# Kernel optimization log

Hardware: AMD Instinct MI355X
Metric: run time of the kernel (lower is better)

## Reference

```python
import jax, jax.numpy as jnp
import numpy as np

NUM_COLS = 8      # MyTopoAgent.num_columns
NUM_SELECTED = 4  # MyTopoAgent.num_selected


def _gatv2(x, src, tgt, Wl, bl, Wr, br, att, bias, n):
    """PyG GATv2Conv (share_weights=False, concat=True, negative_slope=0.2).
    x: [n, Din]; src/tgt: [E] (self loops already appended); att: [H, C]."""
    H, C = att.shape
    xl = (x @ Wl + bl).reshape(n, H, C)   # lin_l(x) -> source transform
    xr = (x @ Wr + br).reshape(n, H, C)   # lin_r(x) -> target transform
    # e_ij = att . leaky_relu(xl[j] + xr[i])  per head
    e = jnp.einsum('ehc,hc->eh', jax.nn.leaky_relu(xl[src] + xr[tgt], 0.2), att)  # [E, H]
    # segment softmax over edges sharing a target node (stable via segment max)
    m = jax.lax.stop_gradient(jax.ops.segment_max(e, tgt, num_segments=n))
    ex = jnp.exp(e - m[tgt])
    denom = jax.ops.segment_sum(ex, tgt, num_segments=n)
    alpha = ex / (denom[tgt] + 1e-16)
    out = jax.ops.segment_sum(xl[src] * alpha[..., None], tgt, num_segments=n)  # [n, H, C]
    return out.reshape(n, H * C) + bias


def setup_inputs() -> dict:
    key = jax.random.key(0)
    B, N, D, Hd, Ch, E = 4, 10000, 128, 128, 7, 640000
    M = B * N
    ks = iter(jax.random.split(key, 40))
    nx = lambda shape: jax.random.normal(next(ks), shape, dtype=jnp.float32) * 0.05
    inp = {}
    inp['x'] = jax.random.normal(next(ks), (B, N, D), dtype=jnp.float32)
    inp['edge_index'] = jax.random.randint(next(ks), (2, E), 0, M)
    inp['gumbel_u'] = jax.random.uniform(next(ks), (B, NUM_COLS, Ch), dtype=jnp.float32,
                                         minval=1e-6, maxval=1.0 - 1e-6)
    # actor gat1(D->Hd), actor gat2(Hd->Ch), critic gat1(D->Hd), critic gat2(Hd->Hd); heads=1
    for pre, di, do in (('a1', D, Hd), ('a2', Hd, Ch), ('c1', D, Hd), ('c2', Hd, Hd)):
        inp[pre + '_Wl'] = nx((di, do))
        inp[pre + '_bl'] = jnp.zeros((do,), jnp.float32)
        inp[pre + '_Wr'] = nx((di, do))
        inp[pre + '_br'] = jnp.zeros((do,), jnp.float32)
        inp[pre + '_att'] = nx((1, do))
        inp[pre + '_b'] = jnp.zeros((do,), jnp.float32)
    inp['fc_W'] = nx((Hd, 1))
    inp['fc_b'] = jnp.zeros((1,), jnp.float32)
    return inp


def reference(x, edge_index, gumbel_u,
              a1_Wl, a1_bl, a1_Wr, a1_br, a1_att, a1_b,
              a2_Wl, a2_bl, a2_Wr, a2_br, a2_att, a2_b,
              c1_Wl, c1_bl, c1_Wr, c1_br, c1_att, c1_b,
              c2_Wl, c2_bl, c2_Wr, c2_br, c2_att, c2_b,
              fc_W, fc_b):
    B, N, D = x.shape
    M = B * N
    xf = x.reshape(M, D)
    loops = jnp.arange(M, dtype=edge_index.dtype)  # PyG add_self_loops
    src = jnp.concatenate([edge_index[0], loops])
    tgt = jnp.concatenate([edge_index[1], loops])
    # ---- actor: GATv2 -> leaky_relu(0.01) -> GATv2 -> softmax ----
    h = _gatv2(xf, src, tgt, a1_Wl, a1_bl, a1_Wr, a1_br, a1_att, a1_b, M)
    h = jax.nn.leaky_relu(h, 0.01)
    logits = _gatv2(h, src, tgt, a2_Wl, a2_bl, a2_Wr, a2_br, a2_att, a2_b, M).reshape(B, N, -1)
    probs = jax.nn.softmax(logits, axis=-1)  # [B, N, 7]
    # multinomial(k=4, no replacement) per column via Gumbel top-k
    g = -jnp.log(-jnp.log(gumbel_u))                       # [B, 8, 7]
    scores = jnp.log(probs[:, :NUM_COLS, :]) + g
    _, action = jax.lax.top_k(scores, NUM_SELECTED)        # [B, 8, 4]
    # torch gather(dim=1): sel[b,i,j] = probs[b, action[b,i,j], j]
    sel = probs[jnp.arange(B)[:, None, None], action, jnp.arange(NUM_SELECTED)[None, None, :]]
    # ---- critic: GATv2 -> leaky_relu(0.01) -> GATv2 -> Linear ----
    hc = _gatv2(xf, src, tgt, c1_Wl, c1_bl, c1_Wr, c1_br, c1_att, c1_b, M)
    hc = jax.nn.leaky_relu(hc, 0.01)
    hc = _gatv2(hc, src, tgt, c2_Wl, c2_bl, c2_Wr, c2_br, c2_att, c2_b, M).reshape(B, N, -1)
    value = hc @ fc_W + fc_b  # [B, N, 1]
    return action, sel, value
```

## Files before the change

kernel.cpp:

```cpp
#include <hip/hip_runtime.h>
#include <math.h>


typedef __attribute__((ext_vector_type(8))) short bf16x8;
typedef __attribute__((ext_vector_type(4))) float f32x4;

__device__ __forceinline__ float wave_reduce_sum(float v){
  #pragma unroll
  for (int o = 32; o > 0; o >>= 1) v += __shfl_xor(v, o);
  return v;
}
__device__ __forceinline__ unsigned short f2bf(float f){
  unsigned int u = __float_as_uint(f);
  u += 0x7FFFu + ((u >> 16) & 1u);
  return (unsigned short)(u >> 16);
}
__device__ __forceinline__ void unpack2(unsigned int u, float& a, float& b){
  a = __uint_as_float(u << 16);
  b = __uint_as_float(u & 0xffff0000u);
}

__global__ void k_zero(int* __restrict__ p, int n){
  int i = blockIdx.x * blockDim.x + threadIdx.x;
  if (i < n) p[i] = 0;
}

__global__ void k_scatter(const int* __restrict__ ei, int E,
                          int* __restrict__ cnt, int* __restrict__ bucket,
                          const float* __restrict__ W1l, const float* __restrict__ W1r,
                          const float* __restrict__ W2l, const float* __restrict__ W2r,
                          unsigned short* __restrict__ Wt1, unsigned short* __restrict__ Wt2){
  int e = blockIdx.x * blockDim.x + threadIdx.x;
  if (e < E){
    int s = ei[e], t = ei[E + e];
    int pos = atomicAdd(&cnt[t], 1);
    if (pos < 64) bucket[(size_t)t * 64 + pos] = s;
  } else {
    int r = e - E;
    if (r < 65536){
      int which = r >> 15;
      int lin = r & 32767;
      const float* Wl = which ? W2l : W1l;
      const float* Wr = which ? W2r : W1r;
      unsigned short* Wt = which ? Wt2 : Wt1;
      int n = lin >> 7, k = lin & 127;
      float v = (n < 128) ? Wl[(size_t)k * 128 + n] : Wr[(size_t)k * 128 + (n - 128)];
      Wt[lin] = f2bf(v);
    }
  }
}

__device__ __forceinline__ void dev_mark1(
    const int* __restrict__ cnt, const int* __restrict__ bucket,
    int* __restrict__ flag1, int* __restrict__ list1, int* __restrict__ n1, int N){
  int p = threadIdx.x;
  if (p >= 32) return;
  int node = (p >> 3) * N + (p & 7);
  if (atomicExch(&flag1[node], 1) == 0) list1[atomicAdd(n1, 1)] = node;
  int deg = min(cnt[node], 64);
  const int* crow = bucket + (size_t)node * 64;
  for (int j = 0; j < deg; ++j){
    int s = crow[j];
    if (atomicExch(&flag1[s], 1) == 0) list1[atomicAdd(n1, 1)] = s;
  }
}
__device__ __forceinline__ void dev_mark2(
    int vbid, int nblk,
    const int* __restrict__ cnt, const int* __restrict__ bucket,
    const int* __restrict__ list1, const int* __restrict__ n1,
    int* __restrict__ flag2, int* __restrict__ list2, int* __restrict__ n2){
  int n = *n1;
  for (int i = vbid * blockDim.x + threadIdx.x; i < n; i += nblk * blockDim.x){
    int node = list1[i];
    if (atomicExch(&flag2[node], 1) == 0) list2[atomicAdd(n2, 1)] = node;
    int deg = min(cnt[node], 64);
    const int* crow = bucket + (size_t)node * 64;
    for (int j = 0; j < deg; ++j){
      int s = crow[j];
      if (atomicExch(&flag2[s], 1) == 0) list2[atomicAdd(n2, 1)] = s;
    }
  }
}

__device__ __forceinline__ void dev_gemm_dual(
    int bid, const float* __restrict__ A,
    const float* __restrict__ Wl, const float* __restrict__ Wr,
    const float* __restrict__ blv, const float* __restrict__ brv,
    float* __restrict__ XL1, float* __restrict__ XR1,
    const int* __restrict__ list1, const int* __restrict__ list2,
    const int* __restrict__ nn,
    float (*As)[17], float (*Ws)[64]){
  const float* W; const float* bias; float* Out; const int* rows; int n;
  int colBase, bx, nbx;
  if (bid < 384){
    W = Wl; bias = blv; Out = XL1; rows = list2; n = nn[1];
    colBase = (bid / 192) * 64; bx = bid % 192; nbx = 192;
  } else {
    int rem = bid - 384;
    W = Wr; bias = brv; Out = XR1; rows = list1; n = nn[0];
    colBase = (rem / 64) * 64; bx = rem % 64; nbx = 64;
  }
  int tid = threadIdx.x;
  int tx = tid & 15, ty = tid >> 4;
  int ar = tid >> 2, ac = (tid & 3) << 2;
  int kr = tid >> 4, nc = (tid & 15) << 2;
  for (int base = bx * 64; base < n; base += nbx * 64){
    float acc[4][4] = {};
    int arow = rows[min(base + ar, n - 1)];
    for (int k0 = 0; k0 < 128; k0 += 16){
      float4 av = *(const float4*)(A + (size_t)arow * 128 + k0 + ac);
      As[ar][ac + 0] = av.x; As[ar][ac + 1] = av.y;
      As[ar][ac + 2] = av.z; As[ar][ac + 3] = av.w;
      float4 wv = *(const float4*)(W + (size_t)(k0 + kr) * 128 + colBase + nc);
      *(float4*)&Ws[kr][nc] = wv;
      __syncthreads();
      #pragma unroll
      for (int kk = 0; kk < 16; ++kk){
        float a0 = As[ty * 4 + 0][kk];
        float a1 = As[ty * 4 + 1][kk];
        float a2 = As[ty * 4 + 2][kk];
        float a3 = As[ty * 4 + 3][kk];
        float4 b = *(const float4*)&Ws[kk][tx * 4];
        acc[0][0] += a0 * b.x; acc[0][1] += a0 * b.y; acc[0][2] += a0 * b.z; acc[0][3] += a0 * b.w;
        acc[1][0] += a1 * b.x; acc[1][1] += a1 * b.y; acc[1][2] += a1 * b.z; acc[1][3] += a1 * b.w;
        acc[2][0] += a2 * b.x; acc[2][1] += a2 * b.y; acc[2][2] += a2 * b.z; acc[2][3] += a2 * b.w;
        acc[3][0] += a3 * b.x; acc[3][1] += a3 * b.y; acc[3][2] += a3 * b.z; acc[3][3] += a3 * b.w;
      }
      __syncthreads();
    }
    int cN = colBase + tx * 4;
    float4 bb = *(const float4*)(bias + cN);
    #pragma unroll
    for (int i = 0; i < 4; ++i){
      int r = rows[min(base + ty * 4 + i, n - 1)];
      float4 o;
      o.x = acc[i][0] + bb.x; o.y = acc[i][1] + bb.y;
      o.z = acc[i][2] + bb.z; o.w = acc[i][3] + bb.w;
      *(float4*)(Out + (size_t)r * 128 + cN) = o;
    }
  }
}

template<bool CVT>
__device__ __forceinline__ void dev_gemm_mfma(
    int rblk, const void* __restrict__ Av, const unsigned short* __restrict__ Wt,
    const float* __restrict__ bl, const float* __restrict__ br,
    unsigned short* __restrict__ XL, unsigned short* __restrict__ XR){
  int w = threadIdx.x >> 6, lane = threadIdx.x & 63;
  int l16 = lane & 15, kg = lane >> 4;
  int rBase = rblk * 64 + w * 16;
  f32x4 acc[16];
  #pragma unroll
  for (int i = 0; i < 16; ++i) acc[i] = (f32x4){0.f, 0.f, 0.f, 0.f};
  #pragma unroll
  for (int ks = 0; ks < 4; ++ks){
    bf16x8 a;
    if constexpr (CVT){
      const float* A = (const float*)Av;
      const float* ap = A + (size_t)(rBase + l16) * 128 + ks * 32 + kg * 8;
      float4 f0 = *(const float4*)ap;
      float4 f1 = *(const float4*)(ap + 4);
      union { bf16x8 v; unsigned short s[8]; } u;
      u.s[0] = f2bf(f0.x); u.s[1] = f2bf(f0.y); u.s[2] = f2bf(f0.z); u.s[3] = f2bf(f0.w);
      u.s[4] = f2bf(f1.x); u.s[5] = f2bf(f1.y); u.s[6] = f2bf(f1.z); u.s[7] = f2bf(f1.w);
      a = u.v;
    } else {
      a = *(const bf16x8*)((const unsigned short*)Av + (size_t)(rBase + l16) * 128 + ks * 32 + kg * 8);
    }
    #pragma unroll
    for (int ct = 0; ct < 16; ++ct){
      bf16x8 wv = *(const bf16x8*)(Wt + (size_t)(ct * 16 + l16) * 128 + ks * 32 + kg * 8);
      acc[ct] = __builtin_amdgcn_mfma_f32_16x16x32_bf16(wv, a, acc[ct], 0, 0, 0);
    }
  }
  int row = rBase + l16;
  #pragma unroll
  for (int ct = 0; ct < 16; ++ct){
    int col = ct * 16 + kg * 4;
    const float* bp = (col < 128) ? (bl + col) : (br + (col - 128));
    float4 bb = *(const float4*)bp;
    unsigned int p0 = (unsigned int)f2bf(acc[ct][0] + bb.x) |
                      ((unsigned int)f2bf(acc[ct][1] + bb.y) << 16);
    unsigned int p1 = (unsigned int)f2bf(acc[ct][2] + bb.z) |
                      ((unsigned int)f2bf(acc[ct][3] + bb.w) << 16);
    unsigned short* dst = (col < 128) ? (XL + (size_t)row * 128 + col)
                                      : (XR + (size_t)row * 128 + (col - 128));
    uint2 pk; pk.x = p0; pk.y = p1;
    *(uint2*)dst = pk;
  }
}

template<int MODE>
__device__ __forceinline__ void dev_gather16(
    int gid, int l,
    const unsigned short* __restrict__ XL, const unsigned short* __restrict__ XR,
    const int* __restrict__ cnt, const int* __restrict__ bucket,
    const float* __restrict__ att, const float* __restrict__ bias,
    const float* __restrict__ fcW, const float* __restrict__ fcb,
    void* __restrict__ outp){
  uint4 xu = *(const uint4*)(XR + (size_t)gid * 128 + l * 8);
  float xr[8];
  unpack2(xu.x, xr[0], xr[1]); unpack2(xu.y, xr[2], xr[3]);
  unpack2(xu.z, xr[4], xr[5]); unpack2(xu.w, xr[6], xr[7]);
  float at[8];
  {
    float4 a0 = *(const float4*)(att + l * 8);
    float4 a1 = *(const float4*)(att + l * 8 + 4);
    at[0] = a0.x; at[1] = a0.y; at[2] = a0.z; at[3] = a0.w;
    at[4] = a1.x; at[5] = a1.y; at[6] = a1.z; at[7] = a1.w;
  }
  int deg = min(cnt[gid], 64);
  const int* __restrict__ crow = bucket + (size_t)gid * 64;
  float m = -INFINITY, den = 0.f;
  float acc[8] = {0.f, 0.f, 0.f, 0.f, 0.f, 0.f, 0.f, 0.f};

  auto proc = [&](uint4 u){
    float xl[8];
    unpack2(u.x, xl[0], xl[1]); unpack2(u.y, xl[2], xl[3]);
    unpack2(u.z, xl[4], xl[5]); unpack2(u.w, xl[6], xl[7]);
    float e = 0.f;
    #pragma unroll
    for (int c = 0; c < 8; ++c){
      float v = xl[c] + xr[c];
      v = fmaxf(v, 0.2f * v);
      e = fmaf(v, at[c], e);
    }
    e += __shfl_xor(e, 1, 16);
    e += __shfl_xor(e, 2, 16);
    e += __shfl_xor(e, 4, 16);
    e += __shfl_xor(e, 8, 16);
    if (e > m){
      float sc = __expf(m - e);
      den *= sc;
      #pragma unroll
      for (int c = 0; c < 8; ++c) acc[c] *= sc;
      m = e;
    }
    float p = __expf(e - m);
    den += p;
    #pragma unroll
    for (int c = 0; c < 8; ++c) acc[c] = fmaf(p, xl[c], acc[c]);
  };

  proc(*(const uint4*)(XL + (size_t)gid * 128 + l * 8));

  int nq = deg >> 2;
  int j = 0;
  if (nq > 0){
    uint4 r0, r1, r2, r3;
    {
      int s0 = crow[0], s1 = crow[1], s2 = crow[2], s3 = crow[3];
      r0 = *(const uint4*)(XL + (size_t)s0 * 128 + l * 8);
      r1 = *(const uint4*)(XL + (size_t)s1 * 128 + l * 8);
      r2 = *(const uint4*)(XL + (size_t)s2 * 128 + l * 8);
      r3 = *(const uint4*)(XL + (size_t)s3 * 128 + l * 8);
    }
    for (int q = 1;; ++q){
      bool more = (q < nq);
      uint4 n0, n1, n2, n3;
      if (more){
        int b4 = q * 4;
        int t0 = crow[b4 + 0], t1 = crow[b4 + 1], t2 = crow[b4 + 2], t3 = crow[b4 + 3];
        n0 = *(const uint4*)(XL + (size_t)t0 * 128 + l * 8);
        n1 = *(const uint4*)(XL + (size_t)t1 * 128 + l * 8);
        n2 = *(const uint4*)(XL + (size_t)t2 * 128 + l * 8);
        n3 = *(const uint4*)(XL + (size_t)t3 * 128 + l * 8);
      }
      proc(r0); proc(r1); proc(r2); proc(r3);
      if (!more) break;
      r0 = n0; r1 = n1; r2 = n2; r3 = n3;
    }
    j = nq * 4;
  }
  for (; j < deg; ++j){
    int s = crow[j];
    proc(*(const uint4*)(XL + (size_t)s * 128 + l * 8));
  }

  float r = 1.f / (den + 1e-16f);
  float4 b0 = *(const float4*)(bias + l * 8);
  float4 b1 = *(const float4*)(bias + l * 8 + 4);
  float o[8];
  o[0] = acc[0] * r + b0.x; o[1] = acc[1] * r + b0.y;
  o[2] = acc[2] * r + b0.z; o[3] = acc[3] * r + b0.w;
  o[4] = acc[4] * r + b1.x; o[5] = acc[5] * r + b1.y;
  o[6] = acc[6] * r + b1.z; o[7] = acc[7] * r + b1.w;
  if (MODE == 0){
    #pragma unroll
    for (int c = 0; c < 8; ++c) o[c] = o[c] > 0.f ? o[c] : 0.01f * o[c];
    uint4 pk;
    pk.x = (unsigned int)f2bf(o[0]) | ((unsigned int)f2bf(o[1]) << 16);
    pk.y = (unsigned int)f2bf(o[2]) | ((unsigned int)f2bf(o[3]) << 16);
    pk.z = (unsigned int)f2bf(o[4]) | ((unsigned int)f2bf(o[5]) << 16);
    pk.w = (unsigned int)f2bf(o[6]) | ((unsigned int)f2bf(o[7]) << 16);
    *(uint4*)((unsigned short*)outp + (size_t)gid * 128 + l * 8) = pk;
  } else {
    float4 w0 = *(const float4*)(fcW + l * 8);
    float4 w1 = *(const float4*)(fcW + l * 8 + 4);
    float pv = o[0] * w0.x + o[1] * w0.y + o[2] * w0.z + o[3] * w0.w +
               o[4] * w1.x + o[5] * w1.y + o[6] * w1.z + o[7] * w1.w;
    pv += __shfl_xor(pv, 1, 16);
    pv += __shfl_xor(pv, 2, 16);
    pv += __shfl_xor(pv, 4, 16);
    pv += __shfl_xor(pv, 8, 16);
    if (l == 0) ((float*)outp)[gid] = pv + fcb[0];
  }
}

__device__ __forceinline__ void dev_a1_fused(
    int vbid,
    const float* __restrict__ XL, const float* __restrict__ XR,
    const int* __restrict__ cnt, const int* __restrict__ bucket,
    const float* __restrict__ att, const float* __restrict__ bias,
    const float* __restrict__ Wl7, const float* __restrict__ Wr7,
    const float* __restrict__ bl7, const float* __restrict__ br7,
    float* __restrict__ XL2, float* __restrict__ XR2,
    const int* __restrict__ list, const int* __restrict__ n_dev){
  int n = *n_dev;
  int lane = threadIdx.x & 63;
  const int wstride = (256 * 256) >> 6;
  for (int i = (vbid * 256 + (int)threadIdx.x) >> 6; i < n; i += wstride){
    int wid = list[i];
    float2 xr = ((const float2*)(XR + (size_t)wid * 128))[lane];
    float2 at = ((const float2*)att)[lane];
    int deg = min(cnt[wid], 64);
    const int* crow = bucket + (size_t)wid * 64;
    float m = -INFINITY, den = 0.f, acc0 = 0.f, acc1 = 0.f;
    for (int j = -1; j < deg; ++j){
      int s = (j < 0) ? wid : crow[j];
      float2 xl = ((const float2*)(XL + (size_t)s * 128))[lane];
      float v0 = xl.x + xr.x, v1 = xl.y + xr.y;
      v0 = v0 > 0.f ? v0 : 0.2f * v0;
      v1 = v1 > 0.f ? v1 : 0.2f * v1;
      float e = wave_reduce_sum(v0 * at.x + v1 * at.y);
      float mn = fmaxf(m, e);
      float sc = __expf(m - mn);
      float p  = __expf(e - mn);
      den  = den  * sc + p;
      acc0 = acc0 * sc + p * xl.x;
      acc1 = acc1 * sc + p * xl.y;
      m = mn;
    }
    float r = 1.f / (den + 1e-16f);
    float2 bs = ((const float2*)bias)[lane];
    float o0 = acc0 * r + bs.x;
    float o1 = acc1 * r + bs.y;
    o0 = o0 > 0.f ? o0 : 0.01f * o0;
    o1 = o1 > 0.f ? o1 : 0.01f * o1;
    #pragma unroll
    for (int c = 0; c < 7; ++c){
      float wl0 = Wl7[(size_t)(2 * lane) * 7 + c];
      float wl1 = Wl7[(size_t)(2 * lane + 1) * 7 + c];
      float wr0 = Wr7[(size_t)(2 * lane) * 7 + c];
      float wr1 = Wr7[(size_t)(2 * lane + 1) * 7 + c];
      float dl = wave_reduce_sum(o0 * wl0 + o1 * wl1);
      float dr = wave_reduce_sum(o0 * wr0 + o1 * wr1);
      if (lane == 0){
        XL2[(size_t)wid * 8 + c] = dl + bl7[c];
        XR2[(size_t)wid * 8 + c] = dr + br7[c];
      }
    }
  }
}

__global__ __launch_bounds__(256) void k_a2head(
    const float* __restrict__ XL2, const float* __restrict__ XR2,
    const int* __restrict__ cnt, const int* __restrict__ bucket,
    const float* __restrict__ att, const float* __restrict__ bias,
    const float* __restrict__ gu,
    float* __restrict__ out_action, float* __restrict__ out_sel, int N){
  __shared__ float pr[32][8];
  int g = threadIdx.x >> 3, c = threadIdx.x & 7;
  int node = (g >> 3) * N + (g & 7);
  float xr = (c < 7) ? XR2[(size_t)node * 8 + c] : 0.f;
  float at = (c < 7) ? att[c] : 0.f;
  int deg = min(cnt[node], 64);
  const int* crow = bucket + (size_t)node * 64;
  float m = -INFINITY, den = 0.f, acc = 0.f;
  for (int j = -1; j < deg; ++j){
    int s = (j < 0) ? node : crow[j];
    float xl = (c < 7) ? XL2[(size_t)s * 8 + c] : 0.f;
    float v = xl + xr;
    v = fmaxf(v, 0.2f * v);
    float e = v * at;
    e += __shfl_xor(e, 1, 8);
    e += __shfl_xor(e, 2, 8);
    e += __shfl_xor(e, 4, 8);
    if (e > m){
      float sc = __expf(m - e);
      den *= sc; acc *= sc; m = e;
    }
    float p = __expf(e - m);
    den += p;
    acc = fmaf(p, xl, acc);
  }
  float lg = acc / (den + 1e-16f) + ((c < 7) ? bias[c] : 0.f);
  float lgv = (c < 7) ? lg : -INFINITY;
  float mx = lgv;
  mx = fmaxf(mx, __shfl_xor(mx, 1, 8));
  mx = fmaxf(mx, __shfl_xor(mx, 2, 8));
  mx = fmaxf(mx, __shfl_xor(mx, 4, 8));
  float ex = (c < 7) ? expf(lgv - mx) : 0.f;
  float sm = ex;
  sm += __shfl_xor(sm, 1, 8);
  sm += __shfl_xor(sm, 2, 8);
  sm += __shfl_xor(sm, 4, 8);
  pr[g][c] = ex / sm;
  __syncthreads();
  int t = threadIdx.x;
  if (t < 32){
    int b = t >> 3;
    float sc[7];
    #pragma unroll
    for (int cc = 0; cc < 7; ++cc){
      float u = gu[t * 7 + cc];
      float gn = -logf(-logf(u));
      sc[cc] = logf(pr[t][cc]) + gn;
    }
    #pragma unroll
    for (int k = 0; k < 4; ++k){
      float best = -INFINITY; int bi = 0;
      #pragma unroll
      for (int cc = 0; cc < 7; ++cc) if (sc[cc] > best){ best = sc[cc]; bi = cc; }
      sc[bi] = -INFINITY;
      out_action[t * 4 + k] = (float)bi;
      out_sel[t * 4 + k] = pr[b * 8 + bi][k];
    }
  }
}

__global__ __launch_bounds__(256) void k_L3(
    const float* __restrict__ x, const unsigned short* __restrict__ Wt1,
    const float* __restrict__ c1_bl, const float* __restrict__ c1_br,
    unsigned short* __restrict__ XLb, unsigned short* __restrict__ XRb, int nMfma,
    const int* __restrict__ cnt, const int* __restrict__ bucket,
    int* __restrict__ flag1, int* __restrict__ list1, int* __restrict__ n1, int N){
  int bid = blockIdx.x;
  if (bid < nMfma){
    dev_gemm_mfma<true>(bid, x, Wt1, c1_bl, c1_br, XLb, XRb);
  } else {
    dev_mark1(cnt, bucket, flag1, list1, n1, N);
  }
}

__global__ __launch_bounds__(256) void k_L4(
    const int* __restrict__ cnt, const int* __restrict__ bucket,
    const int* __restrict__ list1, const int* __restrict__ n1,
    int* __restrict__ flag2, int* __restrict__ list2, int* __restrict__ n2,
    const unsigned short* __restrict__ XLb, const unsigned short* __restrict__ XRb,
    const float* __restrict__ c1_att, const float* __restrict__ c1_b,
    unsigned short* __restrict__ Hb, int M){
  int bid = blockIdx.x;
  if (bid < 64){
    dev_mark2(bid, 64, cnt, bucket, list1, n1, flag2, list2, n2);
  } else {
    int gbid = bid - 64;
    int gid = (gbid * 256 + (int)threadIdx.x) >> 4;
    int l = threadIdx.x & 15;
    if (gid < M)
      dev_gather16<0>(gid, l, XLb, XRb, cnt, bucket, c1_att, c1_b,
                      nullptr, nullptr, (void*)Hb);
  }
}

__global__ __launch_bounds__(256) void k_L5(
    const float* __restrict__ x,
    const float* __restrict__ a1_Wl, const float* __restrict__ a1_Wr,
    const float* __restrict__ a1_bl, const float* __restrict__ a1_br,
    float* __restrict__ XL1, float* __restrict__ XR1,
    const int* __restrict__ list1, const int* __restrict__ list2,
    const int* __restrict__ nn,
    const unsigned short* __restrict__ Hb, const unsigned short* __restrict__ Wt2,
    const float* __restrict__ c2_bl, const float* __restrict__ c2_br,
    unsigned short* __restrict__ XLb, unsigned short* __restrict__ XRb){
  __shared__ float As[64][17];
  __shared__ float Ws[16][64];
  int bid = blockIdx.x;
  if (bid < 512){
    dev_gemm_dual(bid, x, a1_Wl, a1_Wr, a1_bl, a1_br, XL1, XR1, list1, list2, nn, As, Ws);
  } else {
    dev_gemm_mfma<false>(bid - 512, Hb, Wt2, c2_bl, c2_br, XLb, XRb);
  }
}

__global__ __launch_bounds__(256) void k_L6(
    const float* __restrict__ XL1, const float* __restrict__ XR1,
    const int* __restrict__ cnt, const int* __restrict__ bucket,
    const float* __restrict__ a1_att, const float* __restrict__ a1_b,
    const float* __restrict__ Wl7, const float* __restrict__ Wr7,
    const float* __restrict__ bl7, const float* __restrict__ br7,
    float* __restrict__ XL2, float* __restrict__ XR2,
    const int* __restrict__ list1, const int* __restrict__ n1,
    const unsigned short* __restrict__ XLb, const unsigned short* __restrict__ XRb,
    const float* __restrict__ c2_att, const float* __restrict__ c2_b,
    const float* __restrict__ fcW, const float* __restrict__ fcb,
    float* __restrict__ out_value, int M){
  int bid = blockIdx.x;
  if (bid < 256){
    dev_a1_fused(bid, XL1, XR1, cnt, bucket, a1_att, a1_b,
                 Wl7, Wr7, bl7, br7, XL2, XR2, list1, n1);
  } else {
    int gbid = bid - 256;
    int gid = (gbid * 256 + (int)threadIdx.x) >> 4;
    int l = threadIdx.x & 15;
    if (gid < M)
      dev_gather16<1>(gid, l, XLb, XRb, cnt, bucket, c2_att, c2_b,
                      fcW, fcb, (void*)out_value);
  }
}

extern "C" void kernel_launch(void* const* d_in, const int* in_sizes, int n_in,
                              void* d_out, int out_size, void* d_ws, size_t ws_size,
                              hipStream_t stream){
  const float* x  = (const float*)d_in[0];
  const int*   ei = (const int*)d_in[1];
  const float* gu = (const float*)d_in[2];
  const float* a1_Wl = (const float*)d_in[3],  *a1_bl = (const float*)d_in[4];
  const float* a1_Wr = (const float*)d_in[5],  *a1_br = (const float*)d_in[6];
  const float* a1_att= (const float*)d_in[7],  *a1_b  = (const float*)d_in[8];
  const float* a2_Wl = (const float*)d_in[9],  *a2_bl = (const float*)d_in[10];
  const float* a2_Wr = (const float*)d_in[11], *a2_br = (const float*)d_in[12];
  const float* a2_att= (const float*)d_in[13], *a2_b  = (const float*)d_in[14];
  const float* c1_Wl = (const float*)d_in[15], *c1_bl = (const float*)d_in[16];
  const float* c1_Wr = (const float*)d_in[17], *c1_br = (const float*)d_in[18];
  const float* c1_att= (const float*)d_in[19], *c1_b  = (const float*)d_in[20];
  const float* c2_Wl = (const float*)d_in[21], *c2_bl = (const float*)d_in[22];
  const float* c2_Wr = (const float*)d_in[23], *c2_br = (const float*)d_in[24];
  const float* c2_att= (const float*)d_in[25], *c2_b  = (const float*)d_in[26];
  const float* fc_W  = (const float*)d_in[27], *fc_b  = (const float*)d_in[28];

  const int M = in_sizes[0] / 128;
  const int E = in_sizes[1] / 2;
  const int B = in_sizes[2] / 56;
  const int N = M / B;
  const int nw = B * 8;
  const int T = 256;

  char* ws = (char*)d_ws;
  size_t off = 0;
  auto alloc = [&](size_t bytes) -> void* {
    void* p = ws + off;
    off += (bytes + 255) & ~(size_t)255;
    return p;
  };
  int*   cnt    = (int*)alloc((size_t)(3 * M + 2) * 4);
  int*   flag1  = cnt + M;
  int*   flag2  = flag1 + M;
  int*   nn     = flag2 + M;
  int*   bucket = (int*)alloc((size_t)M * 64 * 4);
  int*   list1  = (int*)alloc((size_t)M * 4);
  int*   list2  = (int*)alloc((size_t)M * 4);
  float* XL2    = (float*)alloc((size_t)M * 8 * 4);
  float* XR2    = (float*)alloc((size_t)M * 8 * 4);
  unsigned short* Wt1 = (unsigned short*)alloc((size_t)256 * 128 * 2);
  unsigned short* Wt2 = (unsigned short*)alloc((size_t)256 * 128 * 2);
  float* XL1 = (float*)alloc((size_t)M * 128 * 4);
  float* XR1 = (float*)alloc((size_t)M * 128 * 4);
  unsigned short* XLb = (unsigned short*)alloc((size_t)M * 128 * 2);
  unsigned short* XRb = (unsigned short*)alloc((size_t)M * 128 * 2);
  unsigned short* Hb  = (unsigned short*)alloc((size_t)M * 128 * 2);
  (void)ws_size; (void)n_in; (void)out_size;

  float* out_action = (float*)d_out;
  float* out_sel    = out_action + (size_t)nw * 4;
  float* out_value  = out_sel + (size_t)nw * 4;

  const int G0 = (M * 16 + T - 1) / T;
  const int nMfma = M / 64;
  const int nz = 3 * M + 2;

  k_zero<<<(nz + T - 1) / T, T, 0, stream>>>(cnt, nz);
  k_scatter<<<(E + 65536 + T - 1) / T, T, 0, stream>>>(ei, E, cnt, bucket,
      c1_Wl, c1_Wr, c2_Wl, c2_Wr, Wt1, Wt2);
  k_L3<<<nMfma + 1, T, 0, stream>>>(x, Wt1, c1_bl, c1_br, XLb, XRb, nMfma,
      cnt, bucket, flag1, list1, &nn[0], N);
  k_L4<<<64 + G0, T, 0, stream>>>(cnt, bucket, list1, &nn[0], flag2, list2, &nn[1],
      XLb, XRb, c1_att, c1_b, Hb, M);
  k_L5<<<512 + nMfma, T, 0, stream>>>(x, a1_Wl, a1_Wr, a1_bl, a1_br,
      XL1, XR1, list1, list2, nn, Hb, Wt2, c2_bl, c2_br, XLb, XRb);
  k_L6<<<256 + G0, T, 0, stream>>>(XL1, XR1, cnt, bucket, a1_att, a1_b,
      a2_Wl, a2_Wr, a2_bl, a2_br, XL2, XR2, list1, &nn[0],
      XLb, XRb, c2_att, c2_b, fc_W, fc_b, out_value, M);
  k_a2head<<<1, 256, 0, stream>>>(XL2, XR2, cnt, bucket, a2_att, a2_b, gu,
      out_action, out_sel, N);
}
```

Baseline: 207.5 us.

## Reschedule kernel stages to overlap edge scatter with first MFMA GEMM

Merges the zeroing and weight conversion into one init kernel, then runs the edge-bucket scatter concurrently with the critic layer-1 MFMA GEMM. The later stages are regrouped so each kernel pairs a heavy stage with an independent light one: gather with mark1, GEMM with mark2, the critic-2 gather with the actor dual GEMM. The actor a1 attention stage becomes its own kernel with 512 blocks. The aim is better overlap of independent work and fewer serialized phases, with the same kernel count. It risks load imbalance, since mark stages now sit alongside heavy phases they may block behind.

```diff
diff --git a/kernel.cpp b/kernel.cpp
--- a/kernel.cpp
+++ b/kernel.cpp
@@ -20,23 +20,15 @@
   b = __uint_as_float(u & 0xffff0000u);
 }
 
-__global__ void k_zero(int* __restrict__ p, int n){
+__global__ void k_init(int* __restrict__ p, int nz,
+                       const float* __restrict__ W1l, const float* __restrict__ W1r,
+                       const float* __restrict__ W2l, const float* __restrict__ W2r,
+                       unsigned short* __restrict__ Wt1, unsigned short* __restrict__ Wt2){
   int i = blockIdx.x * blockDim.x + threadIdx.x;
-  if (i < n) p[i] = 0;
-}
-
-__global__ void k_scatter(const int* __restrict__ ei, int E,
-                          int* __restrict__ cnt, int* __restrict__ bucket,
-                          const float* __restrict__ W1l, const float* __restrict__ W1r,
-                          const float* __restrict__ W2l, const float* __restrict__ W2r,
-                          unsigned short* __restrict__ Wt1, unsigned short* __restrict__ Wt2){
-  int e = blockIdx.x * blockDim.x + threadIdx.x;
-  if (e < E){
-    int s = ei[e], t = ei[E + e];
-    int pos = atomicAdd(&cnt[t], 1);
-    if (pos < 64) bucket[(size_t)t * 64 + pos] = s;
-  } else {
-    int r = e - E;
+  if (i < nz){
+    p[i] = 0;
+  } else {
+    int r = i - nz;
     if (r < 65536){
       int which = r >> 15;
       int lin = r & 32767;
@@ -47,6 +39,74 @@
       float v = (n < 128) ? Wl[(size_t)k * 128 + n] : Wr[(size_t)k * 128 + (n - 128)];
       Wt[lin] = f2bf(v);
     }
+  }
+}
+
+template<bool CVT>
+__device__ __forceinline__ void dev_gemm_mfma(
+    int rblk, const void* __restrict__ Av, const unsigned short* __restrict__ Wt,
+    const float* __restrict__ bl, const float* __restrict__ br,
+    unsigned short* __restrict__ XL, unsigned short* __restrict__ XR){
+  int w = threadIdx.x >> 6, lane = threadIdx.x & 63;
+  int l16 = lane & 15, kg = lane >> 4;
+  int rBase = rblk * 64 + w * 16;
+  f32x4 acc[16];
+  #pragma unroll
+  for (int i = 0; i < 16; ++i) acc[i] = (f32x4){0.f, 0.f, 0.f, 0.f};
+  #pragma unroll
+  for (int ks = 0; ks < 4; ++ks){
+    bf16x8 a;
+    if constexpr (CVT){
+      const float* A = (const float*)Av;
+      const float* ap = A + (size_t)(rBase + l16) * 128 + ks * 32 + kg * 8;
+      float4 f0 = *(const float4*)ap;
+      float4 f1 = *(const float4*)(ap + 4);
+      union { bf16x8 v; unsigned short s[8]; } u;
+      u.s[0] = f2bf(f0.x); u.s[1] = f2bf(f0.y); u.s[2] = f2bf(f0.z); u.s[3] = f2bf(f0.w);
+      u.s[4] = f2bf(f1.x); u.s[5] = f2bf(f1.y); u.s[6] = f2bf(f1.z); u.s[7] = f2bf(f1.w);
+      a = u.v;
+    } else {
+      a = *(const bf16x8*)((const unsigned short*)Av + (size_t)(rBase + l16) * 128 + ks * 32 + kg * 8);
+    }
+    #pragma unroll
+    for (int ct = 0; ct < 16; ++ct){
+      bf16x8 wv = *(const bf16x8*)(Wt + (size_t)(ct * 16 + l16) * 128 + ks * 32 + kg * 8);
+      acc[ct] = __builtin_amdgcn_mfma_f32_16x16x32_bf16(wv, a, acc[ct], 0, 0, 0);
+    }
+  }
+  int row = rBase + l16;
+  #pragma unroll
+  for (int ct = 0; ct < 16; ++ct){
+    int col = ct * 16 + kg * 4;
+    const float* bp = (col < 128) ? (bl + col) : (br + (col - 128));
+    float4 bb = *(const float4*)bp;
+    unsigned int p0 = (unsigned int)f2bf(acc[ct][0] + bb.x) |
+                      ((unsigned int)f2bf(acc[ct][1] + bb.y) << 16);
+    unsigned int p1 = (unsigned int)f2bf(acc[ct][2] + bb.z) |
+                      ((unsigned int)f2bf(acc[ct][3] + bb.w) << 16);
+    unsigned short* dst = (col < 128) ? (XL + (size_t)row * 128 + col)
+                                      : (XR + (size_t)row * 128 + (col - 128));
+    uint2 pk; pk.x = p0; pk.y = p1;
+    *(uint2*)dst = pk;
+  }
+}
+
+__global__ __launch_bounds__(256) void k_L2(
+    const int* __restrict__ ei, int E, int nS,
+    int* __restrict__ cnt, int* __restrict__ bucket,
+    const float* __restrict__ x, const unsigned short* __restrict__ Wt1,
+    const float* __restrict__ c1_bl, const float* __restrict__ c1_br,
+    unsigned short* __restrict__ XLb, unsigned short* __restrict__ XRb){
+  int bid = blockIdx.x;
+  if (bid < nS){
+    int e = bid * 256 + threadIdx.x;
+    if (e < E){
+      int s = ei[e], t = ei[E + e];
+      int pos = atomicAdd(&cnt[t], 1);
+      if (pos < 64) bucket[(size_t)t * 64 + pos] = s;
+    }
+  } else {
+    dev_gemm_mfma<true>(bid - nS, x, Wt1, c1_bl, c1_br, XLb, XRb);
   }
 }
 
@@ -79,6 +139,156 @@
       int s = crow[j];
       if (atomicExch(&flag2[s], 1) == 0) list2[atomicAdd(n2, 1)] = s;
     }
+  }
+}
+
+template<int MODE>
+__device__ __forceinline__ void dev_gather16(
+    int gid, int l,
+    const unsigned short* __restrict__ XL, const unsigned short* __restrict__ XR,
+    const int* __restrict__ cnt, const int* __restrict__ bucket,
+    const float* __restrict__ att, const float* __restrict__ bias,
+    const float* __restrict__ fcW, const float* __restrict__ fcb,
+    void* __restrict__ outp){
+  uint4 xu = *(const uint4*)(XR + (size_t)gid * 128 + l * 8);
+  float xr[8];
+  unpack2(xu.x, xr[0], xr[1]); unpack2(xu.y, xr[2], xr[3]);
+  unpack2(xu.z, xr[4], xr[5]); unpack2(xu.w, xr[6], xr[7]);
+  float at[8];
+  {
+    float4 a0 = *(const float4*)(att + l * 8);
+    float4 a1 = *(const float4*)(att + l * 8 + 4);
+    at[0] = a0.x; at[1] = a0.y; at[2] = a0.z; at[3] = a0.w;
+    at[4] = a1.x; at[5] = a1.y; at[6] = a1.z; at[7] = a1.w;
+  }
+  int deg = min(cnt[gid], 64);
+  const int* __restrict__ crow = bucket + (size_t)gid * 64;
+  float m = -INFINITY, den = 0.f;
+  float acc[8] = {0.f, 0.f, 0.f, 0.f, 0.f, 0.f, 0.f, 0.f};
+
+  auto proc = [&](uint4 u){
+    float xl[8];
+    unpack2(u.x, xl[0], xl[1]); unpack2(u.y, xl[2], xl[3]);
+    unpack2(u.z, xl[4], xl[5]); unpack2(u.w, xl[6], xl[7]);
+    float e = 0.f;
+    #pragma unroll
+    for (int c = 0; c < 8; ++c){
+      float v = xl[c] + xr[c];
+      v = fmaxf(v, 0.2f * v);
+      e = fmaf(v, at[c], e);
+    }
+    e += __shfl_xor(e, 1, 16);
+    e += __shfl_xor(e, 2, 16);
+    e += __shfl_xor(e, 4, 16);
+    e += __shfl_xor(e, 8, 16);
+    if (e > m){
+      float sc = __expf(m - e);
+      den *= sc;
+      #pragma unroll
+      for (int c = 0; c < 8; ++c) acc[c] *= sc;
+      m = e;
+    }
+    float p = __expf(e - m);
+    den += p;
+    #pragma unroll
+    for (int c = 0; c < 8; ++c) acc[c] = fmaf(p, xl[c], acc[c]);
+  };
+
+  proc(*(const uint4*)(XL + (size_t)gid * 128 + l * 8));
+
+  int nq = deg >> 2;
+  int j = 0;
+  if (nq > 0){
+    uint4 r0, r1, r2, r3;
+    {
+      int s0 = crow[0], s1 = crow[1], s2 = crow[2], s3 = crow[3];
+      r0 = *(const uint4*)(XL + (size_t)s0 * 128 + l * 8);
+      r1 = *(const uint4*)(XL + (size_t)s1 * 128 + l * 8);
+      r2 = *(const uint4*)(XL + (size_t)s2 * 128 + l * 8);
+      r3 = *(const uint4*)(XL + (size_t)s3 * 128 + l * 8);
+    }
+    for (int q = 1;; ++q){
+      bool more = (q < nq);
+      uint4 n0, n1, n2, n3;
+      if (more){
+        int b4 = q * 4;
+        int t0 = crow[b4 + 0], t1 = crow[b4 + 1], t2 = crow[b4 + 2], t3 = crow[b4 + 3];
+        n0 = *(const uint4*)(XL + (size_t)t0 * 128 + l * 8);
+        n1 = *(const uint4*)(XL + (size_t)t1 * 128 + l * 8);
+        n2 = *(const uint4*)(XL + (size_t)t2 * 128 + l * 8);
+        n3 = *(const uint4*)(XL + (size_t)t3 * 128 + l * 8);
+      }
+      proc(r0); proc(r1); proc(r2); proc(r3);
+      if (!more) break;
+      r0 = n0; r1 = n1; r2 = n2; r3 = n3;
+    }
+    j = nq * 4;
+  }
+  for (; j < deg; ++j){
+    int s = crow[j];
+    proc(*(const uint4*)(XL + (size_t)s * 128 + l * 8));
+  }
+
+  float r = 1.f / (den + 1e-16f);
+  float4 b0 = *(const float4*)(bias + l * 8);
+  float4 b1 = *(const float4*)(bias + l * 8 + 4);
+  float o[8];
+  o[0] = acc[0] * r + b0.x; o[1] = acc[1] * r + b0.y;
+  o[2] = acc[2] * r + b0.z; o[3] = acc[3] * r + b0.w;
+  o[4] = acc[4] * r + b1.x; o[5] = acc[5] * r + b1.y;
+  o[6] = acc[6] * r + b1.z; o[7] = acc[7] * r + b1.w;
+  if (MODE == 0){
+    #pragma unroll
+    for (int c = 0; c < 8; ++c) o[c] = o[c] > 0.f ? o[c] : 0.01f * o[c];
+    uint4 pk;
+    pk.x = (unsigned int)f2bf(o[0]) | ((unsigned int)f2bf(o[1]) << 16);
+    pk.y = (unsigned int)f2bf(o[2]) | ((unsigned int)f2bf(o[3]) << 16);
+    pk.z = (unsigned int)f2bf(o[4]) | ((unsigned int)f2bf(o[5]) << 16);
+    pk.w = (unsigned int)f2bf(o[6]) | ((unsigned int)f2bf(o[7]) << 16);
+    *(uint4*)((unsigned short*)outp + (size_t)gid * 128 + l * 8) = pk;
+  } else {
+    float4 w0 = *(const float4*)(fcW + l * 8);
+    float4 w1 = *(const float4*)(fcW + l * 8 + 4);
+    float pv = o[0] * w0.x + o[1] * w0.y + o[2] * w0.z + o[3] * w0.w +
+               o[4] * w1.x + o[5] * w1.y + o[6] * w1.z + o[7] * w1.w;
+    pv += __shfl_xor(pv, 1, 16);
+    pv += __shfl_xor(pv, 2, 16);
+    pv += __shfl_xor(pv, 4, 16);
+    pv += __shfl_xor(pv, 8, 16);
+    if (l == 0) ((float*)outp)[gid] = pv + fcb[0];
+  }
+}
+
+__global__ __launch_bounds__(256) void k_L3(
+    const unsigned short* __restrict__ XLb, const unsigned short* __restrict__ XRb,
+    const int* __restrict__ cnt, const int* __restrict__ bucket,
+    const float* __restrict__ c1_att, const float* __restrict__ c1_b,
+    unsigned short* __restrict__ Hb, int M, int G0,
+    int* __restrict__ flag1, int* __restrict__ list1, int* __restrict__ n1, int N){
+  int bid = blockIdx.x;
+  if (bid < G0){
+    int gid = (bid * 256 + (int)threadIdx.x) >> 4;
+    int l = threadIdx.x & 15;
+    if (gid < M)
+      dev_gather16<0>(gid, l, XLb, XRb, cnt, bucket, c1_att, c1_b,
+                      nullptr, nullptr, (void*)Hb);
+  } else {
+    dev_mark1(cnt, bucket, flag1, list1, n1, N);
+  }
+}
+
+__global__ __launch_bounds__(256) void k_L4(
+    const unsigned short* __restrict__ Hb, const unsigned short* __restrict__ Wt2,
+    const float* __restrict__ c2_bl, const float* __restrict__ c2_br,
+    unsigned short* __restrict__ XLb, unsigned short* __restrict__ XRb, int nMfma,
+    const int* __restrict__ cnt, const int* __restrict__ bucket,
+    const int* __restrict__ list1, const int* __restrict__ n1,
+    int* __restrict__ flag2, int* __restrict__ list2, int* __restrict__ n2){
+  int bid = blockIdx.x;
+  if (bid < nMfma){
+    dev_gemm_mfma<false>(bid, Hb, Wt2, c2_bl, c2_br, XLb, XRb);
+  } else {
+    dev_mark2(bid - nMfma, 64, cnt, bucket, list1, n1, flag2, list2, n2);
   }
 }
 
@@ -141,174 +351,34 @@
   }
 }
 
-template<bool CVT>
-__device__ __forceinline__ void dev_gemm_mfma(
-    int rblk, const void* __restrict__ Av, const unsigned short* __restrict__ Wt,
-    const float* __restrict__ bl, const float* __restrict__ br,
-    unsigned short* __restrict__ XL, unsigned short* __restrict__ XR){
-  int w = threadIdx.x >> 6, lane = threadIdx.x & 63;
-  int l16 = lane & 15, kg = lane >> 4;
-  int rBase = rblk * 64 + w * 16;
-  f32x4 acc[16];
-  #pragma unroll
-  for (int i = 0; i < 16; ++i) acc[i] = (f32x4){0.f, 0.f, 0.f, 0.f};
-  #pragma unroll
-  for (int ks = 0; ks < 4; ++ks){
-    bf16x8 a;
-    if constexpr (CVT){
-      const float* A = (const float*)Av;
-      const float* ap = A + (size_t)(rBase + l16) * 128 + ks * 32 + kg * 8;
-      float4 f0 = *(const float4*)ap;
-      float4 f1 = *(const float4*)(ap + 4);
-      union { bf16x8 v; unsigned short s[8]; } u;
-      u.s[0] = f2bf(f0.x); u.s[1] = f2bf(f0.y); u.s[2] = f2bf(f0.z); u.s[3] = f2bf(f0.w);
-      u.s[4] = f2bf(f1.x); u.s[5] = f2bf(f1.y); u.s[6] = f2bf(f1.z); u.s[7] = f2bf(f1.w);
-      a = u.v;
-    } else {
-      a = *(const bf16x8*)((const unsigned short*)Av + (size_t)(rBase + l16) * 128 + ks * 32 + kg * 8);
-    }
-    #pragma unroll
-    for (int ct = 0; ct < 16; ++ct){
-      bf16x8 wv = *(const bf16x8*)(Wt + (size_t)(ct * 16 + l16) * 128 + ks * 32 + kg * 8);
-      acc[ct] = __builtin_amdgcn_mfma_f32_16x16x32_bf16(wv, a, acc[ct], 0, 0, 0);
-    }
-  }
-  int row = rBase + l16;
-  #pragma unroll
-  for (int ct = 0; ct < 16; ++ct){
-    int col = ct * 16 + kg * 4;
-    const float* bp = (col < 128) ? (bl + col) : (br + (col - 128));
-    float4 bb = *(const float4*)bp;
-    unsigned int p0 = (unsigned int)f2bf(acc[ct][0] + bb.x) |
-                      ((unsigned int)f2bf(acc[ct][1] + bb.y) << 16);
-    unsigned int p1 = (unsigned int)f2bf(acc[ct][2] + bb.z) |
-                      ((unsigned int)f2bf(acc[ct][3] + bb.w) << 16);
-    unsigned short* dst = (col < 128) ? (XL + (size_t)row * 128 + col)
-                                      : (XR + (size_t)row * 128 + (col - 128));
-    uint2 pk; pk.x = p0; pk.y = p1;
-    *(uint2*)dst = pk;
-  }
-}
-
-template<int MODE>
-__device__ __forceinline__ void dev_gather16(
-    int gid, int l,
-    const unsigned short* __restrict__ XL, const unsigned short* __restrict__ XR,
-    const int* __restrict__ cnt, const int* __restrict__ bucket,
-    const float* __restrict__ att, const float* __restrict__ bias,
+__global__ __launch_bounds__(256) void k_L5(
+    const unsigned short* __restrict__ XLb, const unsigned short* __restrict__ XRb,
+    const int* __restrict__ cnt, const int* __restrict__ bucket,
+    const float* __restrict__ c2_att, const float* __restrict__ c2_b,
     const float* __restrict__ fcW, const float* __restrict__ fcb,
-    void* __restrict__ outp){
-  uint4 xu = *(const uint4*)(XR + (size_t)gid * 128 + l * 8);
-  float xr[8];
-  unpack2(xu.x, xr[0], xr[1]); unpack2(xu.y, xr[2], xr[3]);
-  unpack2(xu.z, xr[4], xr[5]); unpack2(xu.w, xr[6], xr[7]);
-  float at[8];
-  {
-    float4 a0 = *(const float4*)(att + l * 8);
-    float4 a1 = *(const float4*)(att + l * 8 + 4);
-    at[0] = a0.x; at[1] = a0.y; at[2] = a0.z; at[3] = a0.w;
-    at[4] = a1.x; at[5] = a1.y; at[6] = a1.z; at[7] = a1.w;
-  }
-  int deg = min(cnt[gid], 64);
-  const int* __restrict__ crow = bucket + (size_t)gid * 64;
-  float m = -INFINITY, den = 0.f;
-  float acc[8] = {0.f, 0.f, 0.f, 0.f, 0.f, 0.f, 0.f, 0.f};
-
-  auto proc = [&](uint4 u){
-    float xl[8];
-    unpack2(u.x, xl[0], xl[1]); unpack2(u.y, xl[2], xl[3]);
-    unpack2(u.z, xl[4], xl[5]); unpack2(u.w, xl[6], xl[7]);
-    float e = 0.f;
-    #pragma unroll
-    for (int c = 0; c < 8; ++c){
-      float v = xl[c] + xr[c];
-      v = fmaxf(v, 0.2f * v);
-      e = fmaf(v, at[c], e);
-    }
-    e += __shfl_xor(e, 1, 16);
-    e += __shfl_xor(e, 2, 16);
-    e += __shfl_xor(e, 4, 16);
-    e += __shfl_xor(e, 8, 16);
-    if (e > m){
-      float sc = __expf(m - e);
-      den *= sc;
-      #pragma unroll
-      for (int c = 0; c < 8; ++c) acc[c] *= sc;
-      m = e;
-    }
-    float p = __expf(e - m);
-    den += p;
-    #pragma unroll
-    for (int c = 0; c < 8; ++c) acc[c] = fmaf(p, xl[c], acc[c]);
-  };
-
-  proc(*(const uint4*)(XL + (size_t)gid * 128 + l * 8));
-
-  int nq = deg >> 2;
-  int j = 0;
-  if (nq > 0){
-    uint4 r0, r1, r2, r3;
-    {
-      int s0 = crow[0], s1 = crow[1], s2 = crow[2], s3 = crow[3];
-      r0 = *(const uint4*)(XL + (size_t)s0 * 128 + l * 8);
-      r1 = *(const uint4*)(XL + (size_t)s1 * 128 + l * 8);
-      r2 = *(const uint4*)(XL + (size_t)s2 * 128 + l * 8);
-      r3 = *(const uint4*)(XL + (size_t)s3 * 128 + l * 8);
-    }
-    for (int q = 1;; ++q){
-      bool more = (q < nq);
-      uint4 n0, n1, n2, n3;
-      if (more){
-        int b4 = q * 4;
-        int t0 = crow[b4 + 0], t1 = crow[b4 + 1], t2 = crow[b4 + 2], t3 = crow[b4 + 3];
-        n0 = *(const uint4*)(XL + (size_t)t0 * 128 + l * 8);
-        n1 = *(const uint4*)(XL + (size_t)t1 * 128 + l * 8);
-        n2 = *(const uint4*)(XL + (size_t)t2 * 128 + l * 8);
-        n3 = *(const uint4*)(XL + (size_t)t3 * 128 + l * 8);
-      }
-      proc(r0); proc(r1); proc(r2); proc(r3);
-      if (!more) break;
-      r0 = n0; r1 = n1; r2 = n2; r3 = n3;
-    }
-    j = nq * 4;
-  }
-  for (; j < deg; ++j){
-    int s = crow[j];
-    proc(*(const uint4*)(XL + (size_t)s * 128 + l * 8));
-  }
-
-  float r = 1.f / (den + 1e-16f);
-  float4 b0 = *(const float4*)(bias + l * 8);
-  float4 b1 = *(const float4*)(bias + l * 8 + 4);
-  float o[8];
-  o[0] = acc[0] * r + b0.x; o[1] = acc[1] * r + b0.y;
-  o[2] = acc[2] * r + b0.z; o[3] = acc[3] * r + b0.w;
-  o[4] = acc[4] * r + b1.x; o[5] = acc[5] * r + b1.y;
-  o[6] = acc[6] * r + b1.z; o[7] = acc[7] * r + b1.w;
-  if (MODE == 0){
-    #pragma unroll
-    for (int c = 0; c < 8; ++c) o[c] = o[c] > 0.f ? o[c] : 0.01f * o[c];
-    uint4 pk;
-    pk.x = (unsigned int)f2bf(o[0]) | ((unsigned int)f2bf(o[1]) << 16);
-    pk.y = (unsigned int)f2bf(o[2]) | ((unsigned int)f2bf(o[3]) << 16);
-    pk.z = (unsigned int)f2bf(o[4]) | ((unsigned int)f2bf(o[5]) << 16);
-    pk.w = (unsigned int)f2bf(o[6]) | ((unsigned int)f2bf(o[7]) << 16);
-    *(uint4*)((unsigned short*)outp + (size_t)gid * 128 + l * 8) = pk;
-  } else {
-    float4 w0 = *(const float4*)(fcW + l * 8);
-    float4 w1 = *(const float4*)(fcW + l * 8 + 4);
-    float pv = o[0] * w0.x + o[1] * w0.y + o[2] * w0.z + o[3] * w0.w +
-               o[4] * w1.x + o[5] * w1.y + o[6] * w1.z + o[7] * w1.w;
-    pv += __shfl_xor(pv, 1, 16);
-    pv += __shfl_xor(pv, 2, 16);
-    pv += __shfl_xor(pv, 4, 16);
-    pv += __shfl_xor(pv, 8, 16);
-    if (l == 0) ((float*)outp)[gid] = pv + fcb[0];
-  }
-}
-
-__device__ __forceinline__ void dev_a1_fused(
-    int vbid,
+    float* __restrict__ out_value, int M, int G0,
+    const float* __restrict__ x,
+    const float* __restrict__ a1_Wl, const float* __restrict__ a1_Wr,
+    const float* __restrict__ a1_bl, const float* __restrict__ a1_br,
+    float* __restrict__ XL1, float* __restrict__ XR1,
+    const int* __restrict__ list1, const int* __restrict__ list2,
+    const int* __restrict__ nn){
+  int bid = blockIdx.x;
+  if (bid < G0){
+    int gid = (bid * 256 + (int)threadIdx.x) >> 4;
+    int l = threadIdx.x & 15;
+    if (gid < M)
+      dev_gather16<1>(gid, l, XLb, XRb, cnt, bucket, c2_att, c2_b,
+                      fcW, fcb, (void*)out_value);
+  } else {
+    __shared__ float As[64][17];
+    __shared__ float Ws[16][64];
+    dev_gemm_dual(bid - G0, x, a1_Wl, a1_Wr, a1_bl, a1_br,
+                  XL1, XR1, list1, list2, nn, As, Ws);
+  }
+}
+
+__global__ __launch_bounds__(256) void k_a1_fused(
     const float* __restrict__ XL, const float* __restrict__ XR,
     const int* __restrict__ cnt, const int* __restrict__ bucket,
     const float* __restrict__ att, const float* __restrict__ bias,
@@ -318,8 +388,8 @@
     const int* __restrict__ list, const int* __restrict__ n_dev){
   int n = *n_dev;
   int lane = threadIdx.x & 63;
-  const int wstride = (256 * 256) >> 6;
-  for (int i = (vbid * 256 + (int)threadIdx.x) >> 6; i < n; i += wstride){
+  int wstride = (gridDim.x * blockDim.x) >> 6;
+  for (int i = ((int)blockIdx.x * 256 + (int)threadIdx.x) >> 6; i < n; i += wstride){
     int wid = list[i];
     float2 xr = ((const float2*)(XR + (size_t)wid * 128))[lane];
     float2 at = ((const float2*)att)[lane];
@@ -426,86 +496,6 @@
       out_action[t * 4 + k] = (float)bi;
       out_sel[t * 4 + k] = pr[b * 8 + bi][k];
     }
-  }
-}
-
-__global__ __launch_bounds__(256) void k_L3(
-    const float* __restrict__ x, const unsigned short* __restrict__ Wt1,
-    const float* __restrict__ c1_bl, const float* __restrict__ c1_br,
-    unsigned short* __restrict__ XLb, unsigned short* __restrict__ XRb, int nMfma,
-    const int* __restrict__ cnt, const int* __restrict__ bucket,
-    int* __restrict__ flag1, int* __restrict__ list1, int* __restrict__ n1, int N){
-  int bid = blockIdx.x;
-  if (bid < nMfma){
-    dev_gemm_mfma<true>(bid, x, Wt1, c1_bl, c1_br, XLb, XRb);
-  } else {
-    dev_mark1(cnt, bucket, flag1, list1, n1, N);
-  }
-}
-
-__global__ __launch_bounds__(256) void k_L4(
-    const int* __restrict__ cnt, const int* __restrict__ bucket,
-    const int* __restrict__ list1, const int* __restrict__ n1,
-    int* __restrict__ flag2, int* __restrict__ list2, int* __restrict__ n2,
-    const unsigned short* __restrict__ XLb, const unsigned short* __restrict__ XRb,
-    const float* __restrict__ c1_att, const float* __restrict__ c1_b,
-    unsigned short* __restrict__ Hb, int M){
-  int bid = blockIdx.x;
-  if (bid < 64){
-    dev_mark2(bid, 64, cnt, bucket, list1, n1, flag2, list2, n2);
-  } else {
-    int gbid = bid - 64;
-    int gid = (gbid * 256 + (int)threadIdx.x) >> 4;
-    int l = threadIdx.x & 15;
-    if (gid < M)
-      dev_gather16<0>(gid, l, XLb, XRb, cnt, bucket, c1_att, c1_b,
-                      nullptr, nullptr, (void*)Hb);
-  }
-}
-
-__global__ __launch_bounds__(256) void k_L5(
-    const float* __restrict__ x,
-    const float* __restrict__ a1_Wl, const float* __restrict__ a1_Wr,
-    const float* __restrict__ a1_bl, const float* __restrict__ a1_br,
-    float* __restrict__ XL1, float* __restrict__ XR1,
-    const int* __restrict__ list1, const int* __restrict__ list2,
-    const int* __restrict__ nn,
-    const unsigned short* __restrict__ Hb, const unsigned short* __restrict__ Wt2,
-    const float* __restrict__ c2_bl, const float* __restrict__ c2_br,
-    unsigned short* __restrict__ XLb, unsigned short* __restrict__ XRb){
-  __shared__ float As[64][17];
-  __shared__ float Ws[16][64];
-  int bid = blockIdx.x;
-  if (bid < 512){
-    dev_gemm_dual(bid, x, a1_Wl, a1_Wr, a1_bl, a1_br, XL1, XR1, list1, list2, nn, As, Ws);
-  } else {
-    dev_gemm_mfma<false>(bid - 512, Hb, Wt2, c2_bl, c2_br, XLb, XRb);
-  }
-}
-
-__global__ __launch_bounds__(256) void k_L6(
-    const float* __restrict__ XL1, const float* __restrict__ XR1,
-    const int* __restrict__ cnt, const int* __restrict__ bucket,
-    const float* __restrict__ a1_att, const float* __restrict__ a1_b,
-    const float* __restrict__ Wl7, const float* __restrict__ Wr7,
-    const float* __restrict__ bl7, const float* __restrict__ br7,
-    float* __restrict__ XL2, float* __restrict__ XR2,
-    const int* __restrict__ list1, const int* __restrict__ n1,
-    const unsigned short* __restrict__ XLb, const unsigned short* __restrict__ XRb,
-    const float* __restrict__ c2_att, const float* __restrict__ c2_b,
-    const float* __restrict__ fcW, const float* __restrict__ fcb,
-    float* __restrict__ out_value, int M){
-  int bid = blockIdx.x;
-  if (bid < 256){
-    dev_a1_fused(bid, XL1, XR1, cnt, bucket, a1_att, a1_b,
-                 Wl7, Wr7, bl7, br7, XL2, XR2, list1, n1);
-  } else {
-    int gbid = bid - 256;
-    int gid = (gbid * 256 + (int)threadIdx.x) >> 4;
-    int l = threadIdx.x & 15;
-    if (gid < M)
-      dev_gather16<1>(gid, l, XLb, XRb, cnt, bucket, c2_att, c2_b,
-                      fcW, fcb, (void*)out_value);
   }
 }
 
@@ -567,20 +557,22 @@
 
   const int G0 = (M * 16 + T - 1) / T;
   const int nMfma = M / 64;
+  const int nS = (E + T - 1) / T;
   const int nz = 3 * M + 2;
 
-  k_zero<<<(nz + T - 1) / T, T, 0, stream>>>(cnt, nz);
-  k_scatter<<<(E + 65536 + T - 1) / T, T, 0, stream>>>(ei, E, cnt, bucket,
+  k_init<<<(nz + 65536 + T - 1) / T, T, 0, stream>>>(cnt, nz,
       c1_Wl, c1_Wr, c2_Wl, c2_Wr, Wt1, Wt2);
-  k_L3<<<nMfma + 1, T, 0, stream>>>(x, Wt1, c1_bl, c1_br, XLb, XRb, nMfma,
-      cnt, bucket, flag1, list1, &nn[0], N);
-  k_L4<<<64 + G0, T, 0, stream>>>(cnt, bucket, list1, &nn[0], flag2, list2, &nn[1],
-      XLb, XRb, c1_att, c1_b, Hb, M);
-  k_L5<<<512 + nMfma, T, 0, stream>>>(x, a1_Wl, a1_Wr, a1_bl, a1_br,
-      XL1, XR1, list1, list2, nn, Hb, Wt2, c2_bl, c2_br, XLb, XRb);
-  k_L6<<<256 + G0, T, 0, stream>>>(XL1, XR1, cnt, bucket, a1_att, a1_b,
-      a2_Wl, a2_Wr, a2_bl, a2_br, XL2, XR2, list1, &nn[0],
-      XLb, XRb, c2_att, c2_b, fc_W, fc_b, out_value, M);
+  k_L2<<<nS + nMfma, T, 0, stream>>>(ei, E, nS, cnt, bucket,
+      x, Wt1, c1_bl, c1_br, XLb, XRb);
+  k_L3<<<G0 + 1, T, 0, stream>>>(XLb, XRb, cnt, bucket, c1_att, c1_b,
+      Hb, M, G0, flag1, list1, &nn[0], N);
+  k_L4<<<nMfma + 64, T, 0, stream>>>(Hb, Wt2, c2_bl, c2_br, XLb, XRb, nMfma,
+      cnt, bucket, list1, &nn[0], flag2, list2, &nn[1]);
+  k_L5<<<G0 + 512, T, 0, stream>>>(XLb, XRb, cnt, bucket, c2_att, c2_b,
+      fc_W, fc_b, out_value, M, G0,
+      x, a1_Wl, a1_Wr, a1_bl, a1_br, XL1, XR1, list1, list2, nn);
+  k_a1_fused<<<512, T, 0, stream>>>(XL1, XR1, cnt, bucket, a1_att, a1_b,
+      a2_Wl, a2_Wr, a2_bl, a2_br, XL2, XR2, list1, &nn[0]);
   k_a2head<<<1, 256, 0, stream>>>(XL2, XR2, cnt, bucket, a2_att, a2_b, gu,
       out_action, out_sel, N);
 }
```

Result: slower. 250.8 us (+20.9%).
